# Kernel optimization log

Hardware: AMD Instinct MI355X
Metric: run time of the kernel (lower is better)

Reference implementation:

```python
import jax, jax.numpy as jnp
import numpy as np

B, T, D, H, S = 4, 1024, 512, 8, 16
HD = D // H
PRUNING_THRESHOLD = 0.001


def setup_inputs() -> dict:
    key = jax.random.key(0)
    ks = jax.random.split(key, 7)
    x = jax.random.normal(ks[0], (B, T, D), jnp.float32)
    qkv_w = jax.random.normal(ks[1], (3 * D, D), jnp.float32) * (1.0 / np.sqrt(D))
    out_w = jax.random.normal(ks[2], (D, D), jnp.float32) * (1.0 / np.sqrt(D))
    # diverse-ish init for centers (exact init pattern doesn't affect the math being tested)
    base_centers = jax.random.normal(ks[3], (H, S, HD), jnp.float32) * 0.3
    center_deltas = jnp.zeros((H, S, HD), jnp.float32)
    log_scales = jax.random.normal(ks[4], (H, S), jnp.float32) * 0.5 - 0.5
    log_amps = jax.random.normal(ks[5], (H, S), jnp.float32) * 1.0 - 1.5
    movement_param = jnp.asarray(0.05, jnp.float32)
    temperature = jnp.ones((1,), jnp.float32)
    return {
        "x": x, "qkv_w": qkv_w, "out_w": out_w,
        "base_centers": base_centers, "center_deltas": center_deltas,
        "log_scales": log_scales, "log_amps": log_amps,
        "movement_param": movement_param, "temperature": temperature,
    }


def reference(x, qkv_w, out_w, base_centers, center_deltas, log_scales, log_amps,
              movement_param, temperature):
    Bx, Tx, Dx = x.shape
    Hh, Ss, hd = base_centers.shape

    # qkv projection (torch Linear, no bias: y = x @ W.T)
    qkv = (x @ qkv_w.T).reshape(Bx, Tx, 3, Hh, hd)
    q, k, v = qkv[:, :, 0], qkv[:, :, 1], qkv[:, :, 2]  # [B,T,H,hd]

    # effective centers with bounded movement
    move = jax.nn.sigmoid(movement_param) * 0.2
    centers = base_centers + center_deltas * move  # [H,S,hd]

    scales = jnp.clip(jnp.exp(log_scales), 1e-4, 5.0)       # [H,S]
    amps = jnp.clip(jnp.exp(log_amps), 1e-6, 10.0)          # [H,S]
    eff_amps = amps * (amps > PRUNING_THRESHOLD).astype(amps.dtype)
    inv_var = 1.0 / (scales ** 2 + 1e-8)                     # [H,S]

    # squared distances to splat centers: [B,T,H,S]
    q_d2 = jnp.minimum(jnp.sum((q[:, :, :, None, :] - centers[None, None]) ** 2, axis=-1), 100.0)
    k_d2 = jnp.minimum(jnp.sum((k[:, :, :, None, :] - centers[None, None]) ** 2, axis=-1), 100.0)

    q_w = jnp.exp(-0.5 * q_d2 * inv_var) * eff_amps  # [B,T,H,S]
    k_w = jnp.exp(-0.5 * k_d2 * inv_var) * eff_amps  # [B,T,H,S]

    # amplitude-weighted RBF scores: [B,T,T,H]
    logits = jnp.einsum('bihs,bjhs->bijh', q_w, k_w)

    temp = jnp.clip(temperature, 0.01, 10.0)[0]
    attn = jax.nn.softmax(logits / temp + 1e-8, axis=2)  # softmax over j

    out = jnp.einsum('bijh,bjhd->bihd', attn, v).reshape(Bx, Tx, Dx)
    out = out @ out_w.T
    return (out, attn)
```

## Files before the change

kernel.cpp:

```cpp
#include <hip/hip_runtime.h>
#include <hip/hip_bf16.h>

#define B_ 4
#define T_ 1024
#define D_ 512
#define H_ 8
#define S_ 16
#define HD_ 64
#define ITS 8
#define ITW 8
#define PVI 32
#define PVJ 64

typedef short bf16x8 __attribute__((ext_vector_type(8)));
typedef float f32x4m __attribute__((ext_vector_type(4)));

__device__ __forceinline__ unsigned short f2bf(float f) {
  unsigned u = __float_as_uint(f);
  unsigned r = (u + 0x7FFFu + ((u >> 16) & 1u)) >> 16;
  return (unsigned short)r;
}
__device__ __forceinline__ float bf2f(unsigned short h) {
  return __uint_as_float((unsigned)h << 16);
}

__device__ __forceinline__ void split4(const float4 v, ushort4& h, ushort4& l) {
  h.x = f2bf(v.x); l.x = f2bf(v.x - bf2f(h.x));
  h.y = f2bf(v.y); l.y = f2bf(v.y - bf2f(h.y));
  h.z = f2bf(v.z); l.z = f2bf(v.z - bf2f(h.z));
  h.w = f2bf(v.w); l.w = f2bf(v.w - bf2f(h.w));
}

__global__ __launch_bounds__(256) void k_prep(const float* __restrict__ x,
                                              const float* __restrict__ qkv_w,
                                              const float* __restrict__ out_w,
                                              const float* __restrict__ base_centers,
                                              const float* __restrict__ center_deltas,
                                              const float* __restrict__ log_scales,
                                              const float* __restrict__ log_amps,
                                              const float* __restrict__ movement_param,
                                              const float* __restrict__ temperature,
                                              unsigned short* __restrict__ xh,
                                              unsigned short* __restrict__ xl,
                                              unsigned short* __restrict__ wh,
                                              unsigned short* __restrict__ wl,
                                              unsigned short* __restrict__ owh,
                                              unsigned short* __restrict__ owl,
                                              float* __restrict__ centers,
                                              float* __restrict__ inv_var,
                                              float* __restrict__ eff_amps,
                                              float* __restrict__ inv_temp) {
  const int bid = blockIdx.x;
  const int t = threadIdx.x;
  if (bid < 2048) {
    int i = bid * 256 + t;
    float4 v = ((const float4*)x)[i];
    ushort4 h, l; split4(v, h, l);
    ((ushort4*)xh)[i] = h; ((ushort4*)xl)[i] = l;
  } else if (bid < 2816) {
    int i = (bid - 2048) * 256 + t;
    float4 v = ((const float4*)qkv_w)[i];
    ushort4 h, l; split4(v, h, l);
    ((ushort4*)wh)[i] = h; ((ushort4*)wl)[i] = l;
  } else if (bid < 3072) {
    int i = (bid - 2816) * 256 + t;
    float4 v = ((const float4*)out_w)[i];
    ushort4 h, l; split4(v, h, l);
    ((ushort4*)owh)[i] = h; ((ushort4*)owl)[i] = l;
  } else {
    int tid = (bid - 3072) * 256 + t;
    float move = (1.f / (1.f + __expf(-movement_param[0]))) * 0.2f;
    centers[tid] = base_centers[tid] + center_deltas[tid] * move;
    if (tid < H_ * S_) {
      float sc = __expf(log_scales[tid]);
      sc = fminf(fmaxf(sc, 1e-4f), 5.f);
      float am = __expf(log_amps[tid]);
      am = fminf(fmaxf(am, 1e-6f), 10.f);
      inv_var[tid] = 1.f / (sc * sc + 1e-8f);
      eff_amps[tid] = (am > 0.001f) ? am : 0.f;
    }
    if (tid == 0) {
      float tt = fminf(fmaxf(temperature[0], 0.01f), 10.f);
      inv_temp[0] = 1.f / tt;
    }
  }
}

template <int BN>
__global__ __launch_bounds__(256) void gemm_mfma(const unsigned short* __restrict__ Ah,
                                                 const unsigned short* __restrict__ Al,
                                                 const unsigned short* __restrict__ Bh,
                                                 const unsigned short* __restrict__ Bl,
                                                 float* __restrict__ C,
                                                 int M, int N, int K) {
  static_assert(BN == 64, "staging sized for BN=64");
  constexpr int NF = BN / 16;
  const int t = threadIdx.x;
  const int lane = t & 63;
  const int wv = t >> 6;
  const int m0 = blockIdx.y * 128 + wv * 32;
  const int n0 = blockIdx.x * BN;
  const int lr = lane & 15;
  const int kg = lane >> 4;

  __shared__ unsigned short Bsh[64][64];
  __shared__ unsigned short Bsl[64][64];

  const unsigned short* a0h = Ah + (size_t)(m0 + lr) * K + kg * 8;
  const unsigned short* a1h = a0h + (size_t)16 * K;
  const unsigned short* a0l = Al + (size_t)(m0 + lr) * K + kg * 8;
  const unsigned short* a1l = a0l + (size_t)16 * K;

  f32x4m acc[2][NF];
#pragma unroll
  for (int i = 0; i < 2; ++i)
#pragma unroll
    for (int f = 0; f < NF; ++f) {
      f32x4m z = {0.f, 0.f, 0.f, 0.f};
      acc[i][f] = z;
    }

  for (int k0 = 0; k0 < K; k0 += 64) {
    if (k0) __syncthreads();
#pragma unroll
    for (int r2 = 0; r2 < 2; ++r2) {
      int idx = t + r2 * 256;
      int row = idx >> 3, c8 = idx & 7;
      int c8s = c8 ^ (row & 7);
      float4 vh = *(const float4*)(Bh + (size_t)(n0 + row) * K + k0 + c8 * 8);
      float4 vl = *(const float4*)(Bl + (size_t)(n0 + row) * K + k0 + c8 * 8);
      *(float4*)&Bsh[row][c8s * 8] = vh;
      *(float4*)&Bsl[row][c8s * 8] = vl;
    }
    __syncthreads();
#pragma unroll
    for (int S2 = 0; S2 < 2; ++S2) {
      const int kk = k0 + S2 * 32;
      bf16x8 ah0 = *(const bf16x8*)(a0h + kk);
      bf16x8 ah1 = *(const bf16x8*)(a1h + kk);
      bf16x8 al0 = *(const bf16x8*)(a0l + kk);
      bf16x8 al1 = *(const bf16x8*)(a1l + kk);
#pragma unroll
      for (int f = 0; f < NF; ++f) {
        int row = f * 16 + lr;
        int sl = (S2 * 4 + kg) ^ (row & 7);
        bf16x8 vbh = *(const bf16x8*)&Bsh[row][sl * 8];
        bf16x8 vbl = *(const bf16x8*)&Bsl[row][sl * 8];
        acc[0][f] = __builtin_amdgcn_mfma_f32_16x16x32_bf16(al0, vbh, acc[0][f], 0, 0, 0);
        acc[0][f] = __builtin_amdgcn_mfma_f32_16x16x32_bf16(ah0, vbl, acc[0][f], 0, 0, 0);
        acc[0][f] = __builtin_amdgcn_mfma_f32_16x16x32_bf16(ah0, vbh, acc[0][f], 0, 0, 0);
        acc[1][f] = __builtin_amdgcn_mfma_f32_16x16x32_bf16(al1, vbh, acc[1][f], 0, 0, 0);
        acc[1][f] = __builtin_amdgcn_mfma_f32_16x16x32_bf16(ah1, vbl, acc[1][f], 0, 0, 0);
        acc[1][f] = __builtin_amdgcn_mfma_f32_16x16x32_bf16(ah1, vbh, acc[1][f], 0, 0, 0);
      }
    }
  }
#pragma unroll
  for (int i = 0; i < 2; ++i)
#pragma unroll
    for (int f = 0; f < NF; ++f)
#pragma unroll
      for (int r = 0; r < 4; ++r)
        C[(size_t)(m0 + i * 16 + kg * 4 + r) * N + n0 + f * 16 + lr] = acc[i][f][r];
}

template <int BN>
__global__ __launch_bounds__(128) void gemm_mfma2(const unsigned short* __restrict__ Ah,
                                                  const unsigned short* __restrict__ Al,
                                                  const unsigned short* __restrict__ Bh,
                                                  const unsigned short* __restrict__ Bl,
                                                  float* __restrict__ C,
                                                  int M, int N, int K) {
  constexpr int NF = BN / 16;
  const int t = threadIdx.x;
  const int lane = t & 63;
  const int wv = t >> 6;
  const int m0 = blockIdx.y * 64 + wv * 32;
  const int n0 = blockIdx.x * BN;
  const int lr = lane & 15;
  const int kg = lane >> 4;

  const unsigned short* a0h = Ah + (size_t)(m0 + lr) * K + kg * 8;
  const unsigned short* a1h = a0h + (size_t)16 * K;
  const unsigned short* a0l = Al + (size_t)(m0 + lr) * K + kg * 8;
  const unsigned short* a1l = a0l + (size_t)16 * K;
  const unsigned short* bph = Bh + (size_t)(n0 + lr) * K + kg * 8;
  const unsigned short* bpl = Bl + (size_t)(n0 + lr) * K + kg * 8;

  f32x4m acc[2][NF];
#pragma unroll
  for (int i = 0; i < 2; ++i)
#pragma unroll
    for (int f = 0; f < NF; ++f) {
      f32x4m z = {0.f, 0.f, 0.f, 0.f};
      acc[i][f] = z;
    }

  for (int k0 = 0; k0 < K; k0 += 32) {
    bf16x8 ah0 = *(const bf16x8*)(a0h + k0);
    bf16x8 ah1 = *(const bf16x8*)(a1h + k0);
    bf16x8 al0 = *(const bf16x8*)(a0l + k0);
    bf16x8 al1 = *(const bf16x8*)(a1l + k0);
#pragma unroll
    for (int f = 0; f < NF; ++f) {
      bf16x8 vbh = *(const bf16x8*)(bph + (size_t)f * 16 * K + k0);
      bf16x8 vbl = *(const bf16x8*)(bpl + (size_t)f * 16 * K + k0);
      acc[0][f] = __builtin_amdgcn_mfma_f32_16x16x32_bf16(al0, vbh, acc[0][f], 0, 0, 0);
      acc[0][f] = __builtin_amdgcn_mfma_f32_16x16x32_bf16(ah0, vbl, acc[0][f], 0, 0, 0);
      acc[0][f] = __builtin_amdgcn_mfma_f32_16x16x32_bf16(ah0, vbh, acc[0][f], 0, 0, 0);
      acc[1][f] = __builtin_amdgcn_mfma_f32_16x16x32_bf16(al1, vbh, acc[1][f], 0, 0, 0);
      acc[1][f] = __builtin_amdgcn_mfma_f32_16x16x32_bf16(ah1, vbl, acc[1][f], 0, 0, 0);
      acc[1][f] = __builtin_amdgcn_mfma_f32_16x16x32_bf16(ah1, vbh, acc[1][f], 0, 0, 0);
    }
  }
#pragma unroll
  for (int i = 0; i < 2; ++i)
#pragma unroll
    for (int f = 0; f < NF; ++f)
#pragma unroll
      for (int r = 0; r < 4; ++r)
        C[(size_t)(m0 + i * 16 + kg * 4 + r) * N + n0 + f * 16 + lr] = acc[i][f][r];
}

__global__ __launch_bounds__(256) void k_gauss(const float* __restrict__ qkv,
                                               const float* __restrict__ centers,
                                               const float* __restrict__ inv_var,
                                               const float* __restrict__ eff_amps,
                                               const float* __restrict__ inv_temp,
                                               float* __restrict__ qw,
                                               float* __restrict__ kw) {
  int gid = blockIdx.x * blockDim.x + threadIdx.x;
  if (gid >= B_ * T_ * H_ * S_) return;
  int s = gid & 15;
  int h = (gid >> 4) & 7;
  int bt = gid >> 7;
  const float* qrow = qkv + (size_t)bt * 1536 + h * 64;
  const float* krow = qrow + 512;
  const float* c = centers + (h * 16 + s) * 64;
  float qd = 0.f, kd = 0.f;
#pragma unroll
  for (int d = 0; d < 64; d += 4) {
    float4 cv = *(const float4*)(c + d);
    float4 qv = *(const float4*)(qrow + d);
    float4 kv = *(const float4*)(krow + d);
    float t;
    t = qv.x - cv.x; qd += t * t;
    t = qv.y - cv.y; qd += t * t;
    t = qv.z - cv.z; qd += t * t;
    t = qv.w - cv.w; qd += t * t;
    t = kv.x - cv.x; kd += t * t;
    t = kv.y - cv.y; kd += t * t;
    t = kv.z - cv.z; kd += t * t;
    t = kv.w - cv.w; kd += t * t;
  }
  qd = fminf(qd, 100.f);
  kd = fminf(kd, 100.f);
  float iv = inv_var[h * 16 + s];
  float ea = eff_amps[h * 16 + s];
  qw[gid] = __expf(-0.5f * qd * iv) * ea * inv_temp[0];
  kw[gid] = __expf(-0.5f * kd * iv) * ea;
}

__device__ __forceinline__ float dot16(const float4 q[4], const float4 k[4]) {
  return q[0].x * k[0].x + q[0].y * k[0].y + q[0].z * k[0].z + q[0].w * k[0].w +
         q[1].x * k[1].x + q[1].y * k[1].y + q[1].z * k[1].z + q[1].w * k[1].w +
         q[2].x * k[2].x + q[2].y * k[2].y + q[2].z * k[2].z + q[2].w * k[2].w +
         q[3].x * k[3].x + q[3].y * k[3].y + q[3].z * k[3].z + q[3].w * k[3].w;
}

__global__ __launch_bounds__(256, 4) void k_sv(const float* __restrict__ qw_g,
                                               const float* __restrict__ kw_g,
                                               const float* __restrict__ qkv,
                                               float* __restrict__ m_g,
                                               float* __restrict__ is_g,
                                               unsigned short* __restrict__ vth,
                                               unsigned short* __restrict__ vtl) {
  union Sm {
    float red[4][4][2][2];
    float Vl[64][68];
  };
  __shared__ Sm sm;
  const int bid = blockIdx.x;
  const int g = bid / 9;
  const int r = bid - g * 9;
  const int t = threadIdx.x;

  if (r < 8) {
    const int x = g * 8 + r;
    const int ic = x & 127;
    const int h = (x >> 7) & 7;
    const int b = x >> 10;
    const int i0 = ic * ITS;
    const int rp = t & 3;
    const int jl = t >> 2;

    float qwr[2][16], mr[2], sr[2];
#pragma unroll
    for (int e = 0; e < 2; ++e) {
      const float* qp = qw_g + (((size_t)(b * T_ + i0 + rp * 2 + e) * H_ + h) * S_);
#pragma unroll
      for (int s4 = 0; s4 < 4; ++s4) {
        float4 v = *(const float4*)(qp + s4 * 4);
        qwr[e][s4 * 4 + 0] = v.x; qwr[e][s4 * 4 + 1] = v.y;
        qwr[e][s4 * 4 + 2] = v.z; qwr[e][s4 * 4 + 3] = v.w;
      }
      mr[e] = -1e30f; sr[e] = 0.f;
    }
    for (int c = 0; c < T_ / 64; ++c) {
      int j = c * 64 + jl;
      const float* kp = kw_g + ((size_t)(b * T_ + j) * H_ + h) * S_;
      float4 k0 = *(const float4*)(kp);
      float4 k1 = *(const float4*)(kp + 4);
      float4 k2 = *(const float4*)(kp + 8);
      float4 k3 = *(const float4*)(kp + 12);
#pragma unroll
      for (int e = 0; e < 2; ++e) {
        float d = qwr[e][0] * k0.x + qwr[e][1] * k0.y + qwr[e][2] * k0.z + qwr[e][3] * k0.w +
                  qwr[e][4] * k1.x + qwr[e][5] * k1.y + qwr[e][6] * k1.z + qwr[e][7] * k1.w +
                  qwr[e][8] * k2.x + qwr[e][9] * k2.y + qwr[e][10] * k2.z + qwr[e][11] * k2.w +
                  qwr[e][12] * k3.x + qwr[e][13] * k3.y + qwr[e][14] * k3.z + qwr[e][15] * k3.w;
        float mn = fmaxf(mr[e], d);
        sr[e] = sr[e] * __expf(mr[e] - mn) + __expf(d - mn);
        mr[e] = mn;
      }
    }
#pragma unroll
    for (int o = 4; o < 64; o <<= 1) {
#pragma unroll
      for (int e = 0; e < 2; ++e) {
        float m2 = __shfl_xor(mr[e], o);
        float s2 = __shfl_xor(sr[e], o);
        float mn = fmaxf(mr[e], m2);
        sr[e] = sr[e] * __expf(mr[e] - mn) + s2 * __expf(m2 - mn);
        mr[e] = mn;
      }
    }
    int wv = t >> 6;
    if ((t & 63) < 4) {
      sm.red[wv][rp][0][0] = mr[0]; sm.red[wv][rp][0][1] = sr[0];
      sm.red[wv][rp][1][0] = mr[1]; sm.red[wv][rp][1][1] = sr[1];
    }
    __syncthreads();
    if (t < ITS) {
      int rpp = t >> 1, e = t & 1;
      float mf = sm.red[0][rpp][e][0], sf = sm.red[0][rpp][e][1];
#pragma unroll
      for (int w = 1; w < 4; ++w) {
        float m2 = sm.red[w][rpp][e][0], s2 = sm.red[w][rpp][e][1];
        float mn = fmaxf(mf, m2);
        sf = sf * __expf(mf - mn) + s2 * __expf(m2 - mn);
        mf = mn;
      }
      size_t o = (size_t)(b * H_ + h) * T_ + i0 + t;
      m_g[o] = mf;
      is_g[o] = 1.f / sf;
    }
  } else {
    const int id = g;
    const int jc = id & 15;
    const int h = (id >> 4) & 7;
    const int b = id >> 7;
    const int j0 = jc * 64;
    {
      int jj = t >> 2, dqg = t & 3;
      const float* vp = qkv + (size_t)(b * T_ + j0 + jj) * 1536 + 1024 + h * 64 + dqg * 16;
#pragma unroll
      for (int q = 0; q < 4; ++q) {
        float4 v = *(const float4*)(vp + q * 4);
        *(float4*)&sm.Vl[jj][dqg * 16 + q * 4] = v;
      }
    }
    __syncthreads();
    {
      int d = t >> 2, jg = t & 3;
      ushort4 hs[4], ls[4];
#pragma unroll
      for (int q = 0; q < 4; ++q) {
        float f0 = sm.Vl[jg * 16 + q * 4 + 0][d];
        float f1 = sm.Vl[jg * 16 + q * 4 + 1][d];
        float f2 = sm.Vl[jg * 16 + q * 4 + 2][d];
        float f3 = sm.Vl[jg * 16 + q * 4 + 3][d];
        hs[q].x = f2bf(f0); ls[q].x = f2bf(f0 - bf2f(hs[q].x));
        hs[q].y = f2bf(f1); ls[q].y = f2bf(f1 - bf2f(hs[q].y));
        hs[q].z = f2bf(f2); ls[q].z = f2bf(f2 - bf2f(hs[q].z));
        hs[q].w = f2bf(f3); ls[q].w = f2bf(f3 - bf2f(hs[q].w));
      }
      size_t off = ((size_t)(b * H_ + h) * 64 + d) * 1024 + j0 + jg * 16;
#pragma unroll
      for (int q = 0; q < 4; ++q) {
        *(ushort4*)(vth + off + q * 4) = hs[q];
        *(ushort4*)(vtl + off + q * 4) = ls[q];
      }
    }
  }
}

__global__ __launch_bounds__(256, 4) void k_attnw(const float* __restrict__ qw_g,
                                                  const float* __restrict__ kw_g,
                                                  const float* __restrict__ m_g,
                                                  const float* __restrict__ is_g,
                                                  float* __restrict__ attn) {
  const int x = blockIdx.x;
  const int jt = x & 7;
  const int it = (x >> 3) & 127;
  const int b = x >> 10;
  const int i0 = it * ITW;
  const int jbase = jt * 128;
  const int tid = threadIdx.x;

  __shared__ float qw_l[ITW][H_ * S_];
  __shared__ float msl[ITW][H_];
  __shared__ float isl[ITW][H_];
  __shared__ float tile[ITW][H_][68];

  {
    int f = tid * 4;
    int r = f >> 7, c = f & 127;
    *(float4*)&qw_l[r][c] = *(const float4*)(qw_g + ((size_t)(b * T_ + i0 + r) * 128 + c));
  }
  if (tid < 64) {
    int r = tid >> 3, hh = tid & 7;
    size_t o = (size_t)(b * H_ + hh) * T_ + i0 + r;
    msl[r][hh] = m_g[o];
    isl[r][hh] = is_g[o];
  }
  __syncthreads();

  const int h = tid >> 5;
  const int jq = tid & 31;
  const float* kw_b = kw_g + (size_t)b * T_ * (H_ * S_);
  float* attn_b = attn + (size_t)(b * T_ + i0) * (T_ * H_);

  for (int st = 0; st < 2; ++st) {
    const int j0 = jbase + st * 64;
    const float* kp = kw_b + ((size_t)(j0 + jq * 2) * H_ + h) * S_;
    float4 ka[4], kb[4];
    ka[0] = *(const float4*)(kp);       ka[1] = *(const float4*)(kp + 4);
    ka[2] = *(const float4*)(kp + 8);   ka[3] = *(const float4*)(kp + 12);
    kb[0] = *(const float4*)(kp + 128); kb[1] = *(const float4*)(kp + 132);
    kb[2] = *(const float4*)(kp + 136); kb[3] = *(const float4*)(kp + 140);
#pragma unroll
    for (int r = 0; r < ITW; ++r) {
      float4 q4[4];
      q4[0] = *(const float4*)&qw_l[r][h * 16 + 0];
      q4[1] = *(const float4*)&qw_l[r][h * 16 + 4];
      q4[2] = *(const float4*)&qw_l[r][h * 16 + 8];
      q4[3] = *(const float4*)&qw_l[r][h * 16 + 12];
      float la = dot16(q4, ka);
      float lb = dot16(q4, kb);
      float mm = msl[r][h], ii = isl[r][h];
      *(float2*)&tile[r][h][jq * 2] =
          make_float2(__expf(la - mm) * ii, __expf(lb - mm) * ii);
    }
    __syncthreads();
#pragma unroll
    for (int l = 0; l < 4; ++l) {
      int f = (l * 256 + tid) * 4;
      int r = f >> 9;
      int rem = f & 511;
      int jl = rem >> 3;
      int h0 = rem & 7;
      float4 v;
      v.x = tile[r][h0 + 0][jl];
      v.y = tile[r][h0 + 1][jl];
      v.z = tile[r][h0 + 2][jl];
      v.w = tile[r][h0 + 3][jl];
      *(float4*)(attn_b + (size_t)r * (T_ * H_) + (size_t)(j0 + jl) * H_ + h0) = v;
    }
    __syncthreads();
  }
}

__global__ __launch_bounds__(256, 4) void k_pv(const float* __restrict__ qw_g,
                                               const float* __restrict__ kw_g,
                                               const float* __restrict__ m_g,
                                               const float* __restrict__ is_g,
                                               const unsigned short* __restrict__ vth,
                                               const unsigned short* __restrict__ vtl,
                                               unsigned short* __restrict__ oph,
                                               unsigned short* __restrict__ opl) {
  const int bid = blockIdx.x;
  const int xcd = bid & 7;
  const int qq = bid >> 3;
  const int p = xcd * 4 + (qq & 3);
  const int ib = qq >> 2;
  const int b = p >> 3;
  const int h = p & 7;
  const int i0 = ib * PVI;
  const int t = threadIdx.x;
  const int lane = t & 63;
  const int w = t >> 6;
  const int I = w >> 1;
  const int S = w & 1;
  const int lr = lane & 15;
  const int kg = lane >> 4;

  __shared__ float kw_sw[PVJ][16];
  __shared__ float mgs[128][17];

  const int irow = I * 16 + lr;
  float qwr[16];
  {
    const float* qp = qw_g + (((size_t)(b * T_ + i0 + irow) * H_ + h) * S_);
#pragma unroll
    for (int s4 = 0; s4 < 4; ++s4) {
      float4 v = *(const float4*)(qp + s4 * 4);
      qwr[s4 * 4 + 0] = v.x; qwr[s4 * 4 + 1] = v.y;
      qwr[s4 * 4 + 2] = v.z; qwr[s4 * 4 + 3] = v.w;
    }
  }
  float mr = m_g[(size_t)(b * H_ + h) * T_ + i0 + irow];
  float isr = is_g[(size_t)(b * H_ + h) * T_ + i0 + irow];
#pragma unroll
  for (int s = 0; s < 16; ++s) asm volatile("" : "+v"(qwr[s]));
  asm volatile("" : "+v"(mr));
  asm volatile("" : "+v"(isr));

  const unsigned short* vhp = vth + ((size_t)(b * H_ + h) * 64) * 1024;
  const unsigned short* vlp = vtl + ((size_t)(b * H_ + h) * 64) * 1024;

  f32x4m acc[4];
#pragma unroll
  for (int f = 0; f < 4; ++f) { f32x4m z = {0.f, 0.f, 0.f, 0.f}; acc[f] = z; }

  for (int jc = 0; jc < T_ / PVJ; ++jc) {
    const int j0 = jc * PVJ;
    __syncthreads();
    {
      int j = t >> 2, s4g = t & 3;
      float4 v = *(const float4*)(kw_g + (((size_t)(b * T_ + j0 + j) * H_ + h) * S_ + s4g * 4));
      int blk = s4g ^ ((j >> 3) & 3);
      *(float4*)&kw_sw[j][blk * 4] = v;
    }
    __syncthreads();
    union UA { unsigned short s[8]; bf16x8 v; } AH, AL;
#pragma unroll
    for (int u = 0; u < 8; ++u) {
      int jr = S * 32 + kg * 8 + u;
      int g = (jr >> 3) & 3;
      float d = 0.f;
#pragma unroll
      for (int s4 = 0; s4 < 4; ++s4) {
        float4 kv = *(const float4*)&kw_sw[jr][(s4 ^ g) * 4];
        d += qwr[s4 * 4 + 0] * kv.x + qwr[s4 * 4 + 1] * kv.y +
             qwr[s4 * 4 + 2] * kv.z + qwr[s4 * 4 + 3] * kv.w;
      }
      float pv = __expf(d - mr) * isr;
      unsigned short hh = f2bf(pv);
      AH.s[u] = hh;
      AL.s[u] = f2bf(pv - bf2f(hh));
    }
#pragma unroll
    for (int f = 0; f < 4; ++f) {
      size_t voff = (size_t)(f * 16 + lr) * 1024 + j0 + S * 32 + kg * 8;
      bf16x8 BHv = *(const bf16x8*)(vhp + voff);
      bf16x8 BLv = *(const bf16x8*)(vlp + voff);
      acc[f] = __builtin_amdgcn_mfma_f32_16x16x32_bf16(AL.v, BHv, acc[f], 0, 0, 0);
      acc[f] = __builtin_amdgcn_mfma_f32_16x16x32_bf16(AH.v, BLv, acc[f], 0, 0, 0);
      acc[f] = __builtin_amdgcn_mfma_f32_16x16x32_bf16(AH.v, BHv, acc[f], 0, 0, 0);
    }
  }
  __syncthreads();
  if (S == 1) {
    float* dst = &mgs[I * 64 + lane][0];
#pragma unroll
    for (int f = 0; f < 4; ++f)
#pragma unroll
      for (int r = 0; r < 4; ++r) dst[f * 4 + r] = acc[f][r];
  }
  __syncthreads();
  if (S == 0) {
    const float* src = &mgs[I * 64 + lane][0];
#pragma unroll
    for (int f = 0; f < 4; ++f) {
#pragma unroll
      for (int r = 0; r < 4; ++r) {
        float o = acc[f][r] + src[f * 4 + r];
        unsigned short hh = f2bf(o);
        unsigned short ll = f2bf(o - bf2f(hh));
        size_t idx = (size_t)(b * T_ + i0 + I * 16 + kg * 4 + r) * D_ + h * HD_ + f * 16 + lr;
        oph[idx] = hh;
        opl[idx] = ll;
      }
    }
  }
}

extern "C" void kernel_launch(void* const* d_in, const int* in_sizes, int n_in,
                              void* d_out, int out_size, void* d_ws, size_t ws_size,
                              hipStream_t stream) {
  const float* x = (const float*)d_in[0];
  const float* qkv_w = (const float*)d_in[1];
  const float* out_w = (const float*)d_in[2];
  const float* base_c = (const float*)d_in[3];
  const float* deltas = (const float*)d_in[4];
  const float* log_sc = (const float*)d_in[5];
  const float* log_am = (const float*)d_in[6];
  const float* move_p = (const float*)d_in[7];
  const float* temp = (const float*)d_in[8];

  float* out = (float*)d_out;
  float* attn = out + (size_t)B_ * T_ * D_;

  float* ws = (float*)d_ws;
  float* qkv = ws;
  float* qw = qkv + 6291456;
  float* kw = qw + 524288;
  float* centers = kw + 524288;
  float* inv_var = centers + 8192;
  float* eff_amps = inv_var + 128;
  float* inv_temp = eff_amps + 128;
  float* m_g = inv_temp + 4;
  float* is_g = m_g + 32768;
  unsigned short* xh = (unsigned short*)(is_g + 32768);
  unsigned short* xl = xh + 2097152;
  unsigned short* wh = xl + 2097152;
  unsigned short* wl = wh + 786432;
  unsigned short* owh = wl + 786432;
  unsigned short* owl = owh + 262144;
  unsigned short* oph = owl + 262144;
  unsigned short* opl = oph + 2097152;
  unsigned short* vth = opl + 2097152;
  unsigned short* vtl = vth + 2097152;

  k_prep<<<3104, 256, 0, stream>>>(x, qkv_w, out_w, base_c, deltas, log_sc, log_am,
                                   move_p, temp, xh, xl, wh, wl, owh, owl,
                                   centers, inv_var, eff_amps, inv_temp);

  dim3 g1(1536 / 64, 4096 / 128);
  gemm_mfma<64><<<g1, 256, 0, stream>>>(xh, xl, wh, wl, qkv, B_ * T_, 3 * D_, D_);

  k_gauss<<<(B_ * T_ * H_ * S_) / 256, 256, 0, stream>>>(qkv, centers, inv_var,
                                                         eff_amps, inv_temp, qw, kw);
  k_sv<<<4608, 256, 0, stream>>>(qw, kw, qkv, m_g, is_g, vth, vtl);
  k_attnw<<<B_ * (T_ / ITW) * 8, 256, 0, stream>>>(qw, kw, m_g, is_g, attn);
  k_pv<<<B_ * H_ * (T_ / PVI), 256, 0, stream>>>(qw, kw, m_g, is_g, vth, vtl, oph, opl);

  dim3 g2(512 / 32, 4096 / 64);
  gemm_mfma2<32><<<g2, 128, 0, stream>>>(oph, opl, owh, owl, out, B_ * T_, D_, D_);
}
```

Measured before the change: 270.1 us.

## Stage B tiles in LDS for out-proj GEMM, halve gauss threads, split attnw grid

```diff
diff --git a/kernel.cpp b/kernel.cpp
--- a/kernel.cpp
+++ b/kernel.cpp
@@ -171,6 +171,7 @@
                                                   const unsigned short* __restrict__ Bl,
                                                   float* __restrict__ C,
                                                   int M, int N, int K) {
+  static_assert(BN == 32, "staging sized for BN=32");
   constexpr int NF = BN / 16;
   const int t = threadIdx.x;
   const int lane = t & 63;
@@ -180,12 +181,13 @@
   const int lr = lane & 15;
   const int kg = lane >> 4;
 
+  __shared__ unsigned short Bsh[32][64];
+  __shared__ unsigned short Bsl[32][64];
+
   const unsigned short* a0h = Ah + (size_t)(m0 + lr) * K + kg * 8;
   const unsigned short* a1h = a0h + (size_t)16 * K;
   const unsigned short* a0l = Al + (size_t)(m0 + lr) * K + kg * 8;
   const unsigned short* a1l = a0l + (size_t)16 * K;
-  const unsigned short* bph = Bh + (size_t)(n0 + lr) * K + kg * 8;
-  const unsigned short* bpl = Bl + (size_t)(n0 + lr) * K + kg * 8;
 
   f32x4m acc[2][NF];
 #pragma unroll
@@ -196,21 +198,39 @@
       acc[i][f] = z;
     }
 
-  for (int k0 = 0; k0 < K; k0 += 32) {
-    bf16x8 ah0 = *(const bf16x8*)(a0h + k0);
-    bf16x8 ah1 = *(const bf16x8*)(a1h + k0);
-    bf16x8 al0 = *(const bf16x8*)(a0l + k0);
-    bf16x8 al1 = *(const bf16x8*)(a1l + k0);
-#pragma unroll
-    for (int f = 0; f < NF; ++f) {
-      bf16x8 vbh = *(const bf16x8*)(bph + (size_t)f * 16 * K + k0);
-      bf16x8 vbl = *(const bf16x8*)(bpl + (size_t)f * 16 * K + k0);
-      acc[0][f] = __builtin_amdgcn_mfma_f32_16x16x32_bf16(al0, vbh, acc[0][f], 0, 0, 0);
-      acc[0][f] = __builtin_amdgcn_mfma_f32_16x16x32_bf16(ah0, vbl, acc[0][f], 0, 0, 0);
-      acc[0][f] = __builtin_amdgcn_mfma_f32_16x16x32_bf16(ah0, vbh, acc[0][f], 0, 0, 0);
-      acc[1][f] = __builtin_amdgcn_mfma_f32_16x16x32_bf16(al1, vbh, acc[1][f], 0, 0, 0);
-      acc[1][f] = __builtin_amdgcn_mfma_f32_16x16x32_bf16(ah1, vbl, acc[1][f], 0, 0, 0);
-      acc[1][f] = __builtin_amdgcn_mfma_f32_16x16x32_bf16(ah1, vbh, acc[1][f], 0, 0, 0);
+  for (int k0 = 0; k0 < K; k0 += 64) {
+    if (k0) __syncthreads();
+#pragma unroll
+    for (int r2 = 0; r2 < 2; ++r2) {
+      int idx = t + r2 * 128;
+      int row = idx >> 3, c8 = idx & 7;
+      int c8s = c8 ^ (row & 7);
+      float4 vh = *(const float4*)(Bh + (size_t)(n0 + row) * K + k0 + c8 * 8);
+      float4 vl = *(const float4*)(Bl + (size_t)(n0 + row) * K + k0 + c8 * 8);
+      *(float4*)&Bsh[row][c8s * 8] = vh;
+      *(float4*)&Bsl[row][c8s * 8] = vl;
+    }
+    __syncthreads();
+#pragma unroll
+    for (int S2 = 0; S2 < 2; ++S2) {
+      const int kk = k0 + S2 * 32;
+      bf16x8 ah0 = *(const bf16x8*)(a0h + kk);
+      bf16x8 ah1 = *(const bf16x8*)(a1h + kk);
+      bf16x8 al0 = *(const bf16x8*)(a0l + kk);
+      bf16x8 al1 = *(const bf16x8*)(a1l + kk);
+#pragma unroll
+      for (int f = 0; f < NF; ++f) {
+        int row = f * 16 + lr;
+        int sl = (S2 * 4 + kg) ^ (row & 7);
+        bf16x8 vbh = *(const bf16x8*)&Bsh[row][sl * 8];
+        bf16x8 vbl = *(const bf16x8*)&Bsl[row][sl * 8];
+        acc[0][f] = __builtin_amdgcn_mfma_f32_16x16x32_bf16(al0, vbh, acc[0][f], 0, 0, 0);
+        acc[0][f] = __builtin_amdgcn_mfma_f32_16x16x32_bf16(ah0, vbl, acc[0][f], 0, 0, 0);
+        acc[0][f] = __builtin_amdgcn_mfma_f32_16x16x32_bf16(ah0, vbh, acc[0][f], 0, 0, 0);
+        acc[1][f] = __builtin_amdgcn_mfma_f32_16x16x32_bf16(al1, vbh, acc[1][f], 0, 0, 0);
+        acc[1][f] = __builtin_amdgcn_mfma_f32_16x16x32_bf16(ah1, vbl, acc[1][f], 0, 0, 0);
+        acc[1][f] = __builtin_amdgcn_mfma_f32_16x16x32_bf16(ah1, vbh, acc[1][f], 0, 0, 0);
+      }
     }
   }
 #pragma unroll
@@ -230,35 +250,40 @@
                                                float* __restrict__ qw,
                                                float* __restrict__ kw) {
   int gid = blockIdx.x * blockDim.x + threadIdx.x;
-  if (gid >= B_ * T_ * H_ * S_) return;
-  int s = gid & 15;
-  int h = (gid >> 4) & 7;
-  int bt = gid >> 7;
+  int s = gid & 7;
+  int h = (gid >> 3) & 7;
+  int bt = gid >> 6;
   const float* qrow = qkv + (size_t)bt * 1536 + h * 64;
   const float* krow = qrow + 512;
-  const float* c = centers + (h * 16 + s) * 64;
-  float qd = 0.f, kd = 0.f;
+  const float* c0 = centers + (h * 16 + s) * 64;
+  const float* c1 = c0 + 8 * 64;
+  float qd0 = 0.f, kd0 = 0.f, qd1 = 0.f, kd1 = 0.f;
 #pragma unroll
   for (int d = 0; d < 64; d += 4) {
-    float4 cv = *(const float4*)(c + d);
     float4 qv = *(const float4*)(qrow + d);
     float4 kv = *(const float4*)(krow + d);
+    float4 ca = *(const float4*)(c0 + d);
+    float4 cb = *(const float4*)(c1 + d);
     float t;
-    t = qv.x - cv.x; qd += t * t;
-    t = qv.y - cv.y; qd += t * t;
-    t = qv.z - cv.z; qd += t * t;
-    t = qv.w - cv.w; qd += t * t;
-    t = kv.x - cv.x; kd += t * t;
-    t = kv.y - cv.y; kd += t * t;
-    t = kv.z - cv.z; kd += t * t;
-    t = kv.w - cv.w; kd += t * t;
-  }
-  qd = fminf(qd, 100.f);
-  kd = fminf(kd, 100.f);
-  float iv = inv_var[h * 16 + s];
-  float ea = eff_amps[h * 16 + s];
-  qw[gid] = __expf(-0.5f * qd * iv) * ea * inv_temp[0];
-  kw[gid] = __expf(-0.5f * kd * iv) * ea;
+    t = qv.x - ca.x; qd0 += t * t;  t = qv.y - ca.y; qd0 += t * t;
+    t = qv.z - ca.z; qd0 += t * t;  t = qv.w - ca.w; qd0 += t * t;
+    t = kv.x - ca.x; kd0 += t * t;  t = kv.y - ca.y; kd0 += t * t;
+    t = kv.z - ca.z; kd0 += t * t;  t = kv.w - ca.w; kd0 += t * t;
+    t = qv.x - cb.x; qd1 += t * t;  t = qv.y - cb.y; qd1 += t * t;
+    t = qv.z - cb.z; qd1 += t * t;  t = qv.w - cb.w; qd1 += t * t;
+    t = kv.x - cb.x; kd1 += t * t;  t = kv.y - cb.y; kd1 += t * t;
+    t = kv.z - cb.z; kd1 += t * t;  t = kv.w - cb.w; kd1 += t * t;
+  }
+  qd0 = fminf(qd0, 100.f); kd0 = fminf(kd0, 100.f);
+  qd1 = fminf(qd1, 100.f); kd1 = fminf(kd1, 100.f);
+  float it = inv_temp[0];
+  float iv0 = inv_var[h * 16 + s],     ea0 = eff_amps[h * 16 + s];
+  float iv1 = inv_var[h * 16 + s + 8], ea1 = eff_amps[h * 16 + s + 8];
+  size_t base = (size_t)(bt * H_ + h) * S_ + s;
+  qw[base]     = __expf(-0.5f * qd0 * iv0) * ea0 * it;
+  kw[base]     = __expf(-0.5f * kd0 * iv0) * ea0;
+  qw[base + 8] = __expf(-0.5f * qd1 * iv1) * ea1 * it;
+  kw[base + 8] = __expf(-0.5f * kd1 * iv1) * ea1;
 }
 
 __device__ __forceinline__ float dot16(const float4 q[4], const float4 k[4]) {
@@ -401,11 +426,11 @@
                                                   const float* __restrict__ is_g,
                                                   float* __restrict__ attn) {
   const int x = blockIdx.x;
-  const int jt = x & 7;
-  const int it = (x >> 3) & 127;
-  const int b = x >> 10;
+  const int jt = x & 15;
+  const int it = (x >> 4) & 127;
+  const int b = x >> 11;
   const int i0 = it * ITW;
-  const int jbase = jt * 128;
+  const int j0 = jt * 64;
   const int tid = threadIdx.x;
 
   __shared__ float qw_l[ITW][H_ * S_];
@@ -431,43 +456,39 @@
   const float* kw_b = kw_g + (size_t)b * T_ * (H_ * S_);
   float* attn_b = attn + (size_t)(b * T_ + i0) * (T_ * H_);
 
-  for (int st = 0; st < 2; ++st) {
-    const int j0 = jbase + st * 64;
-    const float* kp = kw_b + ((size_t)(j0 + jq * 2) * H_ + h) * S_;
-    float4 ka[4], kb[4];
-    ka[0] = *(const float4*)(kp);       ka[1] = *(const float4*)(kp + 4);
-    ka[2] = *(const float4*)(kp + 8);   ka[3] = *(const float4*)(kp + 12);
-    kb[0] = *(const float4*)(kp + 128); kb[1] = *(const float4*)(kp + 132);
-    kb[2] = *(const float4*)(kp + 136); kb[3] = *(const float4*)(kp + 140);
-#pragma unroll
-    for (int r = 0; r < ITW; ++r) {
-      float4 q4[4];
-      q4[0] = *(const float4*)&qw_l[r][h * 16 + 0];
-      q4[1] = *(const float4*)&qw_l[r][h * 16 + 4];
-      q4[2] = *(const float4*)&qw_l[r][h * 16 + 8];
-      q4[3] = *(const float4*)&qw_l[r][h * 16 + 12];
-      float la = dot16(q4, ka);
-      float lb = dot16(q4, kb);
-      float mm = msl[r][h], ii = isl[r][h];
-      *(float2*)&tile[r][h][jq * 2] =
-          make_float2(__expf(la - mm) * ii, __expf(lb - mm) * ii);
-    }
-    __syncthreads();
-#pragma unroll
-    for (int l = 0; l < 4; ++l) {
-      int f = (l * 256 + tid) * 4;
-      int r = f >> 9;
-      int rem = f & 511;
-      int jl = rem >> 3;
-      int h0 = rem & 7;
-      float4 v;
-      v.x = tile[r][h0 + 0][jl];
-      v.y = tile[r][h0 + 1][jl];
-      v.z = tile[r][h0 + 2][jl];
-      v.w = tile[r][h0 + 3][jl];
-      *(float4*)(attn_b + (size_t)r * (T_ * H_) + (size_t)(j0 + jl) * H_ + h0) = v;
-    }
-    __syncthreads();
+  const float* kp = kw_b + ((size_t)(j0 + jq * 2) * H_ + h) * S_;
+  float4 ka[4], kb[4];
+  ka[0] = *(const float4*)(kp);       ka[1] = *(const float4*)(kp + 4);
+  ka[2] = *(const float4*)(kp + 8);   ka[3] = *(const float4*)(kp + 12);
+  kb[0] = *(const float4*)(kp + 128); kb[1] = *(const float4*)(kp + 132);
+  kb[2] = *(const float4*)(kp + 136); kb[3] = *(const float4*)(kp + 140);
+#pragma unroll
+  for (int r = 0; r < ITW; ++r) {
+    float4 q4[4];
+    q4[0] = *(const float4*)&qw_l[r][h * 16 + 0];
+    q4[1] = *(const float4*)&qw_l[r][h * 16 + 4];
+    q4[2] = *(const float4*)&qw_l[r][h * 16 + 8];
+    q4[3] = *(const float4*)&qw_l[r][h * 16 + 12];
+    float la = dot16(q4, ka);
+    float lb = dot16(q4, kb);
+    float mm = msl[r][h], ii = isl[r][h];
+    *(float2*)&tile[r][h][jq * 2] =
+        make_float2(__expf(la - mm) * ii, __expf(lb - mm) * ii);
+  }
+  __syncthreads();
+#pragma unroll
+  for (int l = 0; l < 4; ++l) {
+    int f = (l * 256 + tid) * 4;
+    int r = f >> 9;
+    int rem = f & 511;
+    int jl = rem >> 3;
+    int h0 = rem & 7;
+    float4 v;
+    v.x = tile[r][h0 + 0][jl];
+    v.y = tile[r][h0 + 1][jl];
+    v.z = tile[r][h0 + 2][jl];
+    v.w = tile[r][h0 + 3][jl];
+    *(float4*)(attn_b + (size_t)r * (T_ * H_) + (size_t)(j0 + jl) * H_ + h0) = v;
   }
 }
 
@@ -630,10 +651,10 @@
   dim3 g1(1536 / 64, 4096 / 128);
   gemm_mfma<64><<<g1, 256, 0, stream>>>(xh, xl, wh, wl, qkv, B_ * T_, 3 * D_, D_);
 
-  k_gauss<<<(B_ * T_ * H_ * S_) / 256, 256, 0, stream>>>(qkv, centers, inv_var,
-                                                         eff_amps, inv_temp, qw, kw);
+  k_gauss<<<(B_ * T_ * H_ * 8) / 256, 256, 0, stream>>>(qkv, centers, inv_var,
+                                                        eff_amps, inv_temp, qw, kw);
   k_sv<<<4608, 256, 0, stream>>>(qw, kw, qkv, m_g, is_g, vth, vtl);
-  k_attnw<<<B_ * (T_ / ITW) * 8, 256, 0, stream>>>(qw, kw, m_g, is_g, attn);
+  k_attnw<<<B_ * (T_ / ITW) * 16, 256, 0, stream>>>(qw, kw, m_g, is_g, attn);
   k_pv<<<B_ * H_ * (T_ / PVI), 256, 0, stream>>>(qw, kw, m_g, is_g, vth, vtl, oph, opl);
 
   dim3 g2(512 / 32, 4096 / 64);
```

Measured after the change: 253.4 us. 6.2% less time.
